# Optimization experiments

Measured on AMD Instinct MI355X. Metric: run time of the kernel, lower is better.

The kernel has to match this reference:

```python
import jax, jax.numpy as jnp
import numpy as np

B, S, D_IN, D_OUT = 4, 2048, 1024, 1024

def setup_inputs() -> dict:
    key = jax.random.key(0)
    kx, kq, kk, kv = jax.random.split(key, 4)
    sc = 1.0 / np.sqrt(D_IN)
    x = jax.random.normal(kx, (B, S, D_IN), dtype=jnp.float32)
    Wq = jax.random.normal(kq, (D_IN, D_OUT), dtype=jnp.float32) * sc
    Wk = jax.random.normal(kk, (D_IN, D_OUT), dtype=jnp.float32) * sc
    Wv = jax.random.normal(kv, (D_IN, D_OUT), dtype=jnp.float32) * sc
    return {"x": x, "Wq": Wq, "Wk": Wk, "Wv": Wv}

def reference(x, Wq, Wk, Wv):
    # x: [B,S,Din]; projections to [B,S,Dout]
    q = jnp.einsum('bsd,de->bse', x, Wq)
    k = jnp.einsum('bsd,de->bse', x, Wk)
    v = jnp.einsum('bsd,de->bse', x, Wv)
    scale = 1.0 / jnp.sqrt(jnp.asarray(q.shape[-1], q.dtype))
    scores = jnp.einsum('bqe,bke->bqk', q, k) * scale  # [B,S,S]
    causal = jnp.tril(jnp.ones((scores.shape[-2], scores.shape[-1]), dtype=bool))
    scores = jnp.where(causal, scores, -jnp.inf)
    attn = jax.nn.softmax(scores, axis=-1)
    # dropout p=0.0 -> identity
    return jnp.einsum('bqk,bke->bqe', attn, v)
```

## Files before the change

### kernel.cpp

```cpp
#include <hip/hip_runtime.h>

#define SEQ 2048
#define DIM 1024

typedef __attribute__((ext_vector_type(8))) __bf16 bf16x8;
typedef __attribute__((ext_vector_type(4))) float f32x4;

typedef __attribute__((address_space(1))) unsigned char gu8_t;
typedef __attribute__((address_space(3))) unsigned char lu8_t;

__device__ __forceinline__ void async_copy16(const void* g, void* l) {
  __builtin_amdgcn_global_load_lds((gu8_t*)g, (lu8_t*)l, 16, 0, 0);
}

__device__ __forceinline__ ushort f2bf(float f) {
  union { float f; unsigned u; } v;
  v.f = f;
  unsigned r = v.u + 0x7FFFu + ((v.u >> 16) & 1u);
  return (ushort)(r >> 16);
}

__global__ void detect_dtype(const unsigned* __restrict__ words,
                             int* __restrict__ flag) {
  const int t = threadIdx.x;
  int hits = 0;
  for (int i = 0; i < 64; i++) {
    const unsigned w = words[t * 64 + i];
    const unsigned b = (w >> 8) & 0x7Fu;
    hits += (b >= 0x3Bu && b <= 0x42u) ? 1 : 0;
  }
#pragma unroll
  for (int o = 32; o > 0; o >>= 1) hits += __shfl_xor(hits, o, 64);
  if (t == 0) *flag = (hits > 2048) ? 1 : 0;
}

__global__ void convert_x(const void* __restrict__ in,
                          ushort* __restrict__ out,
                          const int* __restrict__ flag, int n8) {
  const int i = blockIdx.x * 256 + threadIdx.x;
  if (i >= n8) return;
  if (*flag) {
    reinterpret_cast<uint4*>(out)[i] = reinterpret_cast<const uint4*>(in)[i];
  } else {
    const float4* f = reinterpret_cast<const float4*>(in);
    const float4 a = f[2 * i], b = f[2 * i + 1];
    ushort4 lo, hi;
    lo.x = f2bf(a.x); lo.y = f2bf(a.y); lo.z = f2bf(a.z); lo.w = f2bf(a.w);
    hi.x = f2bf(b.x); hi.y = f2bf(b.y); hi.z = f2bf(b.z); hi.w = f2bf(b.w);
    reinterpret_cast<ushort4*>(out)[2 * i] = lo;
    reinterpret_cast<ushort4*>(out)[2 * i + 1] = hi;
  }
}

__global__ void transpose_w(const void* __restrict__ w0,
                            const void* __restrict__ w1,
                            const void* __restrict__ w2,
                            ushort* __restrict__ out,
                            const int* __restrict__ flag) {
  __shared__ ushort tile[64][68];
  const int z = blockIdx.z;
  const void* in = (z == 0) ? w0 : (z == 1) ? w1 : w2;
  ushort* op = out + (size_t)z * 1024 * 1024;
  const int c0 = blockIdx.x * 64, r0 = blockIdx.y * 64;
  const int t = threadIdx.x;
  if (*flag) {
    const ushort* ip = (const ushort*)in;
#pragma unroll
    for (int i = 0; i < 4; i++) {
      const int lin = i * 256 + t;
      const int r = lin >> 4, c4 = (lin & 15) << 2;
      const ushort4 v = *reinterpret_cast<const ushort4*>(
          ip + (size_t)(r0 + r) * 1024 + c0 + c4);
      tile[r][c4 + 0] = v.x; tile[r][c4 + 1] = v.y;
      tile[r][c4 + 2] = v.z; tile[r][c4 + 3] = v.w;
    }
  } else {
    const float* ip = (const float*)in;
#pragma unroll
    for (int i = 0; i < 4; i++) {
      const int lin = i * 256 + t;
      const int r = lin >> 4, c4 = (lin & 15) << 2;
      const float4 v = *reinterpret_cast<const float4*>(
          ip + (size_t)(r0 + r) * 1024 + c0 + c4);
      tile[r][c4 + 0] = f2bf(v.x); tile[r][c4 + 1] = f2bf(v.y);
      tile[r][c4 + 2] = f2bf(v.z); tile[r][c4 + 3] = f2bf(v.w);
    }
  }
  __syncthreads();
#pragma unroll
  for (int i = 0; i < 4; i++) {
    const int lin = i * 256 + t;
    const int c = lin >> 4, r4 = (lin & 15) << 2;
    ushort4 v;
    v.x = tile[r4 + 0][c]; v.y = tile[r4 + 1][c];
    v.z = tile[r4 + 2][c]; v.w = tile[r4 + 3][c];
    *reinterpret_cast<ushort4*>(op + (size_t)(c0 + c) * 1024 + r0 + r4) = v;
  }
}

__global__ void transpose_bf16(const ushort* __restrict__ in,
                               ushort* __restrict__ out, int R, int C,
                               long inZ, long outZ) {
  __shared__ ushort tile[64][68];
  const ushort* ip = in + (size_t)blockIdx.z * inZ;
  ushort* op = out + (size_t)blockIdx.z * outZ;
  const int c0 = blockIdx.x * 64, r0 = blockIdx.y * 64;
  const int t = threadIdx.x;
#pragma unroll
  for (int i = 0; i < 4; i++) {
    const int lin = i * 256 + t;
    const int r = lin >> 4, c4 = (lin & 15) << 2;
    const ushort4 v =
        *reinterpret_cast<const ushort4*>(ip + (size_t)(r0 + r) * C + c0 + c4);
    tile[r][c4 + 0] = v.x; tile[r][c4 + 1] = v.y;
    tile[r][c4 + 2] = v.z; tile[r][c4 + 3] = v.w;
  }
  __syncthreads();
#pragma unroll
  for (int i = 0; i < 4; i++) {
    const int lin = i * 256 + t;
    const int c = lin >> 4, r4 = (lin & 15) << 2;
    ushort4 v;
    v.x = tile[r4 + 0][c]; v.y = tile[r4 + 1][c];
    v.z = tile[r4 + 2][c]; v.w = tile[r4 + 3][c];
    *reinterpret_cast<ushort4*>(op + (size_t)(c0 + c) * R + r0 + r4) = v;
  }
}

template <int EPI, int OUTK, int TRI, int CK, int CBAL, int M, int N, int K,
          long AZ, long BZ, long CZ>
__global__ __launch_bounds__(256, 4) void gemm_t(
    const ushort* __restrict__ A, const ushort* __restrict__ Bt,
    void* __restrict__ Cv, const int* __restrict__ flag,
    float* __restrict__ lsum, float scale0, float scale1) {
  __shared__ ushort lA[128 * 32];
  __shared__ ushort lB[128 * 32];
  __shared__ float lsh[(EPI == 2) ? 128 : 1];

  constexpr int MT = M / 128;
  const int nT = gridDim.x;
  const int id = blockIdx.y * nT + blockIdx.x;
  const int xcd = id & 7;
  const int loc = id >> 3;
  const int nt = loc % nT;
  const int mt = CBAL ? ((loc / nT == 0) ? xcd : (MT - 1 - xcd))
                      : (xcd + ((loc / nT) << 3));
  const int n0 = nt * 128;
  const int m0 = mt * 128;
  if (TRI && n0 > m0 + 127) return;

  const int z = blockIdx.z;
  const ushort* Ab = A + (size_t)z * AZ;
  const ushort* Bb = Bt + (size_t)z * BZ;

  const int t = threadIdx.x;
  const int lane = t & 63;
  const int w = t >> 6;
  const int wm = (w >> 1) * 64;
  const int wn = (w & 1) * 64;
  const int quad = lane >> 4;
  const int l15 = lane & 15;

  if constexpr (EPI == 2) {
    if (t < 128) lsh[t] = 1.0f / lsum[(size_t)z * M + m0 + t];
  }

  f32x4 acc[4][4] = {};

  const int kEnd = CK ? ((m0 + 128 < K) ? (m0 + 128) : K) : K;

  const int idx0 = t;
  const int idx1 = t + 256;
  const int rowA0 = idx0 >> 2, colA0 = (idx0 & 3) << 3;
  const int rowA1 = idx1 >> 2, colA1 = (idx1 & 3) << 3;

  for (int k0 = 0; k0 < kEnd; k0 += 32) {
    __syncthreads();
    async_copy16(Ab + (size_t)(m0 + rowA0) * K + k0 + colA0, lA + idx0 * 8);
    async_copy16(Ab + (size_t)(m0 + rowA1) * K + k0 + colA1, lA + idx1 * 8);
    async_copy16(Bb + (size_t)(n0 + rowA0) * K + k0 + colA0, lB + idx0 * 8);
    async_copy16(Bb + (size_t)(n0 + rowA1) * K + k0 + colA1, lB + idx1 * 8);
    __syncthreads();

    bf16x8 af[4], bfr[4];
#pragma unroll
    for (int mi = 0; mi < 4; mi++)
      af[mi] = *(const bf16x8*)(lA + (wm + mi * 16 + l15) * 32 + quad * 8);
#pragma unroll
    for (int ni = 0; ni < 4; ni++)
      bfr[ni] = *(const bf16x8*)(lB + (wn + ni * 16 + l15) * 32 + quad * 8);
#pragma unroll
    for (int mi = 0; mi < 4; mi++)
#pragma unroll
      for (int ni = 0; ni < 4; ni++)
        acc[mi][ni] = __builtin_amdgcn_mfma_f32_16x16x32_bf16(
            af[mi], bfr[ni], acc[mi][ni], 0, 0, 0);
  }

  const size_t zc = (size_t)z * CZ;

  if constexpr (EPI == 1) {
    ushort* C = (ushort*)Cv + zc;
    float* ls = lsum + (size_t)z * M;
#pragma unroll
    for (int mi = 0; mi < 4; mi++)
#pragma unroll
      for (int r = 0; r < 4; r++) {
        const int row = m0 + wm + mi * 16 + quad * 4 + r;
        float partial = 0.0f;
#pragma unroll
        for (int ni = 0; ni < 4; ni++) {
          const int col = n0 + wn + ni * 16 + l15;
          const float ev = (col <= row) ? __expf(acc[mi][ni][r]) : 0.0f;
          C[(size_t)row * N + col] = f2bf(ev);
          partial += ev;
        }
#pragma unroll
        for (int o = 1; o < 16; o <<= 1) partial += __shfl_xor(partial, o, 64);
        if (l15 == 0) atomicAdd(&ls[row], partial);
      }
    return;
  } else {
    const float scale = (z == 0) ? scale0 : scale1;
    const bool storeBf = (OUTK == 1) || (OUTK == 2 && *flag != 0);
#pragma unroll
    for (int mi = 0; mi < 4; mi++)
#pragma unroll
      for (int ni = 0; ni < 4; ni++)
#pragma unroll
        for (int r = 0; r < 4; r++) {
          const int lrow = wm + mi * 16 + quad * 4 + r;
          const int row = m0 + lrow;
          const int col = n0 + wn + ni * 16 + l15;
          const float sc = (EPI == 2) ? lsh[lrow] : scale;
          const float vv = acc[mi][ni][r] * sc;
          if (storeBf) {
            ushort* C = (ushort*)Cv + zc;
            C[(size_t)row * N + col] = f2bf(vv);
          } else {
            float* C = (float*)Cv + zc;
            C[(size_t)row * N + col] = vv;
          }
        }
  }
}

using ProjT = void (*)(const ushort*, const ushort*, void*, const int*,
                       float*, float, float);

extern "C" void kernel_launch(void* const* d_in, const int* in_sizes, int n_in,
                              void* d_out, int out_size, void* d_ws,
                              size_t ws_size, hipStream_t stream) {
  char* ws = (char*)d_ws;
  const size_t MB = 1024 * 1024;
  int* flag = (int*)ws;
  ushort* wt = (ushort*)(ws + 1 * MB);
  ushort* xb = (ushort*)(ws + 7 * MB);
  ushort* q = (ushort*)(ws + 23 * MB);
  ushort* kk = (ushort*)(ws + 39 * MB);
  ushort* v = (ushort*)(ws + 55 * MB);
  ushort* vt = (ushort*)(ws + 71 * MB);
  ushort* sc = (ushort*)(ws + 87 * MB);
  float* lsum = (float*)(ws + 119 * MB);
  (void)kk;

  detect_dtype<<<dim3(1), 64, 0, stream>>>((const unsigned*)d_in[0], flag);

  hipMemsetAsync(lsum, 0, 4 * SEQ * sizeof(float), stream);

  convert_x<<<dim3(4096), 256, 0, stream>>>(d_in[0], xb, flag,
                                            (8192 * 1024) / 8);

  transpose_w<<<dim3(16, 16, 3), 256, 0, stream>>>(d_in[1], d_in[2], d_in[3],
                                                   wt, flag);

  gemm_t<0, 1, 0, 0, 0, 8192, 1024, 1024, 0L, 1024L * 1024, 8192L * 1024>
      <<<dim3(8, 64, 3), 256, 0, stream>>>(xb, wt, (void*)q, flag, nullptr,
                                           0.03125f, 1.0f);

  transpose_bf16<<<dim3(16, 32, 4), 256, 0, stream>>>(
      v, vt, 2048, 1024, (long)SEQ * DIM, (long)DIM * SEQ);

  gemm_t<1, 1, 1, 0, 1, 2048, 2048, 1024, (long)SEQ * DIM, (long)SEQ * DIM,
         (long)SEQ * SEQ>
      <<<dim3(16, 16, 4), 256, 0, stream>>>(q, kk, (void*)sc, flag, lsum,
                                            1.0f, 1.0f);

  gemm_t<2, 2, 0, 1, 1, 2048, 1024, 2048, (long)SEQ * SEQ, (long)DIM * SEQ,
         (long)SEQ * DIM>
      <<<dim3(8, 16, 4), 256, 0, stream>>>(sc, vt, d_out, flag, lsum, 1.0f,
                                           1.0f);
}
```

Measured before the change: 260.2 us.

## Compute V transposed directly via Wv^T·X^T GEMM and fuse prep kernels

```diff
diff --git a/kernel.cpp b/kernel.cpp
--- a/kernel.cpp
+++ b/kernel.cpp
@@ -20,50 +20,58 @@
   return (ushort)(r >> 16);
 }
 
-__global__ void detect_dtype(const unsigned* __restrict__ words,
-                             int* __restrict__ flag) {
+__global__ void detect_and_zero(const unsigned* __restrict__ words,
+                                int* __restrict__ flag,
+                                float* __restrict__ lsum) {
   const int t = threadIdx.x;
-  int hits = 0;
-  for (int i = 0; i < 64; i++) {
-    const unsigned w = words[t * 64 + i];
-    const unsigned b = (w >> 8) & 0x7Fu;
-    hits += (b >= 0x3Bu && b <= 0x42u) ? 1 : 0;
-  }
-#pragma unroll
-  for (int o = 32; o > 0; o >>= 1) hits += __shfl_xor(hits, o, 64);
-  if (t == 0) *flag = (hits > 2048) ? 1 : 0;
-}
-
-__global__ void convert_x(const void* __restrict__ in,
-                          ushort* __restrict__ out,
-                          const int* __restrict__ flag, int n8) {
-  const int i = blockIdx.x * 256 + threadIdx.x;
-  if (i >= n8) return;
-  if (*flag) {
-    reinterpret_cast<uint4*>(out)[i] = reinterpret_cast<const uint4*>(in)[i];
-  } else {
-    const float4* f = reinterpret_cast<const float4*>(in);
-    const float4 a = f[2 * i], b = f[2 * i + 1];
-    ushort4 lo, hi;
-    lo.x = f2bf(a.x); lo.y = f2bf(a.y); lo.z = f2bf(a.z); lo.w = f2bf(a.w);
-    hi.x = f2bf(b.x); hi.y = f2bf(b.y); hi.z = f2bf(b.z); hi.w = f2bf(b.w);
-    reinterpret_cast<ushort4*>(out)[2 * i] = lo;
-    reinterpret_cast<ushort4*>(out)[2 * i + 1] = hi;
-  }
-}
-
-__global__ void transpose_w(const void* __restrict__ w0,
-                            const void* __restrict__ w1,
-                            const void* __restrict__ w2,
-                            ushort* __restrict__ out,
-                            const int* __restrict__ flag) {
+  for (int i = t; i < 4 * SEQ; i += 256) lsum[i] = 0.0f;
+  if (t < 64) {
+    int hits = 0;
+    for (int i = 0; i < 64; i++) {
+      const unsigned w = words[t * 64 + i];
+      const unsigned b = (w >> 8) & 0x7Fu;
+      hits += (b >= 0x3Bu && b <= 0x42u) ? 1 : 0;
+    }
+#pragma unroll
+    for (int o = 32; o > 0; o >>= 1) hits += __shfl_xor(hits, o, 64);
+    if (t == 0) *flag = (hits > 2048) ? 1 : 0;
+  }
+}
+
+__global__ void prep(const void* __restrict__ xin, const void* __restrict__ w0,
+                     const void* __restrict__ w1, const void* __restrict__ w2,
+                     ushort* __restrict__ xb, ushort* __restrict__ wt,
+                     const int* __restrict__ flag) {
   __shared__ ushort tile[64][68];
-  const int z = blockIdx.z;
+  const int bid = blockIdx.x;
+  const int t = threadIdx.x;
+  const int bf = *flag;
+
+  if (bid < 4096) {
+    const int i = bid * 256 + t;
+    if (bf) {
+      reinterpret_cast<uint4*>(xb)[i] =
+          reinterpret_cast<const uint4*>(xin)[i];
+    } else {
+      const float4* f = reinterpret_cast<const float4*>(xin);
+      const float4 a = f[2 * i], b = f[2 * i + 1];
+      ushort4 lo, hi;
+      lo.x = f2bf(a.x); lo.y = f2bf(a.y); lo.z = f2bf(a.z); lo.w = f2bf(a.w);
+      hi.x = f2bf(b.x); hi.y = f2bf(b.y); hi.z = f2bf(b.z); hi.w = f2bf(b.w);
+      reinterpret_cast<ushort4*>(xb)[2 * i] = lo;
+      reinterpret_cast<ushort4*>(xb)[2 * i + 1] = hi;
+    }
+    return;
+  }
+
+  const int rem = bid - 4096;
+  const int z = rem >> 8;
+  const int within = rem & 255;
+  const int c0 = (within & 15) * 64, r0 = (within >> 4) * 64;
   const void* in = (z == 0) ? w0 : (z == 1) ? w1 : w2;
-  ushort* op = out + (size_t)z * 1024 * 1024;
-  const int c0 = blockIdx.x * 64, r0 = blockIdx.y * 64;
-  const int t = threadIdx.x;
-  if (*flag) {
+  ushort* op = wt + (size_t)z * 1024 * 1024;
+
+  if (bf) {
     const ushort* ip = (const ushort*)in;
 #pragma unroll
     for (int i = 0; i < 4; i++) {
@@ -98,37 +106,8 @@
   }
 }
 
-__global__ void transpose_bf16(const ushort* __restrict__ in,
-                               ushort* __restrict__ out, int R, int C,
-                               long inZ, long outZ) {
-  __shared__ ushort tile[64][68];
-  const ushort* ip = in + (size_t)blockIdx.z * inZ;
-  ushort* op = out + (size_t)blockIdx.z * outZ;
-  const int c0 = blockIdx.x * 64, r0 = blockIdx.y * 64;
-  const int t = threadIdx.x;
-#pragma unroll
-  for (int i = 0; i < 4; i++) {
-    const int lin = i * 256 + t;
-    const int r = lin >> 4, c4 = (lin & 15) << 2;
-    const ushort4 v =
-        *reinterpret_cast<const ushort4*>(ip + (size_t)(r0 + r) * C + c0 + c4);
-    tile[r][c4 + 0] = v.x; tile[r][c4 + 1] = v.y;
-    tile[r][c4 + 2] = v.z; tile[r][c4 + 3] = v.w;
-  }
-  __syncthreads();
-#pragma unroll
-  for (int i = 0; i < 4; i++) {
-    const int lin = i * 256 + t;
-    const int c = lin >> 4, r4 = (lin & 15) << 2;
-    ushort4 v;
-    v.x = tile[r4 + 0][c]; v.y = tile[r4 + 1][c];
-    v.z = tile[r4 + 2][c]; v.w = tile[r4 + 3][c];
-    *reinterpret_cast<ushort4*>(op + (size_t)(c0 + c) * R + r0 + r4) = v;
-  }
-}
-
-template <int EPI, int OUTK, int TRI, int CK, int CBAL, int M, int N, int K,
-          long AZ, long BZ, long CZ>
+template <int EPI, int OUTK, int TRI, int CK, int CBAL, int SWIZ, int M,
+          int N, int K, long AZ, long BZ, long CZ, long BRS>
 __global__ __launch_bounds__(256, 4) void gemm_t(
     const ushort* __restrict__ A, const ushort* __restrict__ Bt,
     void* __restrict__ Cv, const int* __restrict__ flag,
@@ -142,9 +121,16 @@
   const int id = blockIdx.y * nT + blockIdx.x;
   const int xcd = id & 7;
   const int loc = id >> 3;
-  const int nt = loc % nT;
-  const int mt = CBAL ? ((loc / nT == 0) ? xcd : (MT - 1 - xcd))
-                      : (xcd + ((loc / nT) << 3));
+  int nt, mt;
+  if constexpr (SWIZ == 1) {
+    const int ng = nT >> 3;
+    nt = xcd * ng + loc % ng;
+    mt = loc / ng;
+  } else {
+    nt = loc % nT;
+    mt = CBAL ? ((loc / nT == 0) ? xcd : (MT - 1 - xcd))
+              : (xcd + ((loc / nT) << 3));
+  }
   const int n0 = nt * 128;
   const int m0 = mt * 128;
   if (TRI && n0 > m0 + 127) return;
@@ -178,8 +164,8 @@
     __syncthreads();
     async_copy16(Ab + (size_t)(m0 + rowA0) * K + k0 + colA0, lA + idx0 * 8);
     async_copy16(Ab + (size_t)(m0 + rowA1) * K + k0 + colA1, lA + idx1 * 8);
-    async_copy16(Bb + (size_t)(n0 + rowA0) * K + k0 + colA0, lB + idx0 * 8);
-    async_copy16(Bb + (size_t)(n0 + rowA1) * K + k0 + colA1, lB + idx1 * 8);
+    async_copy16(Bb + (size_t)(n0 + rowA0) * BRS + k0 + colA0, lB + idx0 * 8);
+    async_copy16(Bb + (size_t)(n0 + rowA1) * BRS + k0 + colA1, lB + idx1 * 8);
     __syncthreads();
 
     bf16x8 af[4], bfr[4];
@@ -245,9 +231,6 @@
   }
 }
 
-using ProjT = void (*)(const ushort*, const ushort*, void*, const int*,
-                       float*, float, float);
-
 extern "C" void kernel_launch(void* const* d_in, const int* in_sizes, int n_in,
                               void* d_out, int out_size, void* d_ws,
                               size_t ws_size, hipStream_t stream) {
@@ -258,36 +241,34 @@
   ushort* xb = (ushort*)(ws + 7 * MB);
   ushort* q = (ushort*)(ws + 23 * MB);
   ushort* kk = (ushort*)(ws + 39 * MB);
-  ushort* v = (ushort*)(ws + 55 * MB);
-  ushort* vt = (ushort*)(ws + 71 * MB);
-  ushort* sc = (ushort*)(ws + 87 * MB);
-  float* lsum = (float*)(ws + 119 * MB);
+  ushort* vt = (ushort*)(ws + 55 * MB);
+  ushort* sc = (ushort*)(ws + 71 * MB);
+  float* lsum = (float*)(ws + 103 * MB);
   (void)kk;
 
-  detect_dtype<<<dim3(1), 64, 0, stream>>>((const unsigned*)d_in[0], flag);
-
-  hipMemsetAsync(lsum, 0, 4 * SEQ * sizeof(float), stream);
-
-  convert_x<<<dim3(4096), 256, 0, stream>>>(d_in[0], xb, flag,
-                                            (8192 * 1024) / 8);
-
-  transpose_w<<<dim3(16, 16, 3), 256, 0, stream>>>(d_in[1], d_in[2], d_in[3],
-                                                   wt, flag);
-
-  gemm_t<0, 1, 0, 0, 0, 8192, 1024, 1024, 0L, 1024L * 1024, 8192L * 1024>
-      <<<dim3(8, 64, 3), 256, 0, stream>>>(xb, wt, (void*)q, flag, nullptr,
+  detect_and_zero<<<dim3(1), 256, 0, stream>>>((const unsigned*)d_in[0], flag,
+                                               lsum);
+
+  prep<<<dim3(4864), 256, 0, stream>>>(d_in[0], d_in[1], d_in[2], d_in[3], xb,
+                                       wt, flag);
+
+  gemm_t<0, 1, 0, 0, 0, 0, 8192, 1024, 1024, 0L, 1024L * 1024, 8192L * 1024,
+         1024L>
+      <<<dim3(8, 64, 2), 256, 0, stream>>>(xb, wt, (void*)q, flag, nullptr,
                                            0.03125f, 1.0f);
 
-  transpose_bf16<<<dim3(16, 32, 4), 256, 0, stream>>>(
-      v, vt, 2048, 1024, (long)SEQ * DIM, (long)DIM * SEQ);
-
-  gemm_t<1, 1, 1, 0, 1, 2048, 2048, 1024, (long)SEQ * DIM, (long)SEQ * DIM,
-         (long)SEQ * SEQ>
+  gemm_t<0, 1, 0, 0, 0, 1, 1024, 8192, 1024, 0L, 0L, 0L, 1024L>
+      <<<dim3(64, 8, 1), 256, 0, stream>>>(wt + 2 * 1024 * 1024, xb,
+                                           (void*)vt, flag, nullptr, 1.0f,
+                                           1.0f);
+
+  gemm_t<1, 1, 1, 0, 1, 0, 2048, 2048, 1024, (long)SEQ * DIM, (long)SEQ * DIM,
+         (long)SEQ * SEQ, (long)DIM>
       <<<dim3(16, 16, 4), 256, 0, stream>>>(q, kk, (void*)sc, flag, lsum,
                                             1.0f, 1.0f);
 
-  gemm_t<2, 2, 0, 1, 1, 2048, 1024, 2048, (long)SEQ * SEQ, (long)DIM * SEQ,
-         (long)SEQ * DIM>
+  gemm_t<2, 2, 0, 1, 1, 0, 2048, 1024, 2048, (long)SEQ * SEQ, 2048L,
+         (long)SEQ * DIM, 8192L>
       <<<dim3(8, 16, 4), 256, 0, stream>>>(sc, vt, d_out, flag, lsum, 1.0f,
                                            1.0f);
 }
```

New measurement: 257.0 us. About the same (-1.2%).
